# Kernel optimization log

Hardware: AMD Instinct MI355X
Metric: run time of the kernel (lower is better)

Reference implementation:

```python
import jax, jax.numpy as jnp
import numpy as np
import math

N_NODES = 4096
NUM_FEATURES = 500
NHID = 256
RATIO = 0.75


def _build_adj(x):
    # Faithful vectorization of get_threshold/get_edge_index:
    # t = 0.5 * max_{i,j} ||x_i - x_j||^2 ; directed edges (src=i -> dst=j) for j>i with d2<t.
    # Dense adjacency A[dst, src] (jit-friendly; edge count is data-dependent in the original).
    sq = jnp.sum(x * x, axis=1)
    d2 = sq[:, None] + sq[None, :] - 2.0 * (x @ x.T)  # [N,N] squared distances
    t = 0.5 * jnp.max(d2)
    N = x.shape[0]
    lower = jnp.tril(jnp.ones((N, N), dtype=bool), k=-1)  # entry [j,i], j>i
    return jnp.where(lower & (d2 < t), 1.0, 0.0).astype(x.dtype)


def _gcn(A, x, W, b):
    # PyG GCNConv: add self-loops, symmetric normalization D^-1/2 (A+I) D^-1/2, then @ (xW) + b
    N = A.shape[0]
    Ah = A + jnp.eye(N, dtype=A.dtype)
    dis = jax.lax.rsqrt(jnp.sum(Ah, axis=1))  # deg >= 1 due to self loops
    norm = (dis[:, None] * Ah) * dis[None, :]
    return norm @ (x @ W) + b


def _sag_pool(A, x, Wr, Wn, bn, k):
    # SAGPooling with default GraphConv scorer: score = sum-aggr(neighbors)@Wn + bn + x@Wr
    score = jnp.tanh(((A @ x) @ Wn + bn + x @ Wr)[:, 0])  # [N]
    vals, perm = jax.lax.top_k(score, k)  # top ceil(ratio*N) nodes, descending
    xp = x[perm] * vals[:, None]
    Ap = A[perm][:, perm]  # filter edges to surviving nodes
    return Ap, xp


def _readout(x):
    # single graph (batch=None -> all zeros): [gmp, gap] -> [1, 2*nhid]
    return jnp.concatenate([jnp.max(x, axis=0), jnp.mean(x, axis=0)])[None, :]


def setup_inputs() -> dict:
    key = jax.random.key(0)
    ks = jax.random.split(key, 16)
    s = 0.02
    inp = {
        "feature": jax.random.normal(ks[0], (N_NODES, NUM_FEATURES), jnp.float32),
        "img_info": jax.random.normal(ks[1], (N_NODES, 6), jnp.float32),
        "W_pos": jax.random.normal(ks[2], (6, 12), jnp.float32) * s,
        "b_pos": jnp.zeros((12,), jnp.float32),
        "W1": jax.random.normal(ks[3], (512, NHID), jnp.float32) * s,
        "b1": jnp.zeros((NHID,), jnp.float32),
        "W2": jax.random.normal(ks[4], (NHID, NHID), jnp.float32) * s,
        "b2": jnp.zeros((NHID,), jnp.float32),
        "W3": jax.random.normal(ks[5], (NHID, NHID), jnp.float32) * s,
        "b3": jnp.zeros((NHID,), jnp.float32),
        "Wr1": jax.random.normal(ks[6], (NHID, 1), jnp.float32) * s,
        "Wn1": jax.random.normal(ks[7], (NHID, 1), jnp.float32) * s,
        "bs1": jnp.zeros((1,), jnp.float32),
        "Wr2": jax.random.normal(ks[8], (NHID, 1), jnp.float32) * s,
        "Wn2": jax.random.normal(ks[9], (NHID, 1), jnp.float32) * s,
        "bs2": jnp.zeros((1,), jnp.float32),
        "Wr3": jax.random.normal(ks[10], (NHID, 1), jnp.float32) * s,
        "Wn3": jax.random.normal(ks[11], (NHID, 1), jnp.float32) * s,
        "bs3": jnp.zeros((1,), jnp.float32),
    }
    return inp


def reference(feature, img_info, W_pos, b_pos, W1, b1, W2, b2, W3, b3,
              Wr1, Wn1, bs1, Wr2, Wn2, bs2, Wr3, Wn3, bs3):
    pos = jax.nn.relu(img_info @ W_pos + b_pos)          # [N,12]
    feat = jnp.concatenate([feature, pos], axis=1)       # [N,512]
    N = feat.shape[0]
    k1 = math.ceil(RATIO * N)
    k2 = math.ceil(RATIO * k1)
    k3 = math.ceil(RATIO * k2)

    A = _build_adj(feat)

    x = jax.nn.relu(_gcn(A, feat, W1, b1))
    A, x = _sag_pool(A, x, Wr1, Wn1, bs1, k1)
    x1 = _readout(x)

    x = jax.nn.relu(_gcn(A, x, W2, b2))
    A, x = _sag_pool(A, x, Wr2, Wn2, bs2, k2)
    x2 = _readout(x)

    x = jax.nn.relu(_gcn(A, x, W3, b3))
    A, x = _sag_pool(A, x, Wr3, Wn3, bs3, k3)
    x3 = _readout(x)

    return x1 + x2 + x3  # [1, 2*NHID]
```

## Files before the change

kernel.cpp:

```cpp
#include <hip/hip_runtime.h>
#include <hip/hip_bf16.h>
#include <math.h>

typedef __hip_bfloat16 bf16;
typedef unsigned short ushort;
typedef unsigned int uint;
typedef unsigned long long ull;
static __device__ __forceinline__ float b2f(bf16 x){ return __bfloat162float(x); }

static __device__ __forceinline__ float ldf(const void* p, int i, int isbf){
    return isbf ? b2f(((const bf16*)p)[i]) : ((const float*)p)[i];
}
static __device__ __forceinline__ ushort f2b(float x){
    return __bfloat16_as_ushort(__float2bfloat16(x));
}
static __device__ __forceinline__ uint fcode(float v){
    uint u = __float_as_uint(v);
    return (u & 0x80000000u) ? ~u : (u | 0x80000000u);
}
static __device__ __forceinline__ float fdecode(uint c){
    uint u = (c & 0x80000000u) ? (c & 0x7FFFFFFFu) : ~c;
    return __uint_as_float(u);
}

#define NN    4096
#define FEAT0 500
#define DIN   512
#define NH    256
#define KL1   3072
#define KL2   2304
#define KL3   1728
#define EDGE_CAP 786432u

typedef __attribute__((ext_vector_type(8)))  short v8s;
typedef __attribute__((ext_vector_type(16))) float v16f;

static __device__ __forceinline__ void detect_bf16(const void* p, int n, int t,
        uint* flag){
    if (t < 256 && t < n){
        uint e = ((uint)((const ushort*)p)[t] >> 7) & 0xFFu;
        if (e >= 135u) atomicAnd(flag, 0u);
    }
}

struct DtIn { const void* p[19]; int n[19]; };
__global__ __launch_bounds__(512) void k_prep(DtIn da,
        ushort* __restrict__ Xb, float* __restrict__ sq, ushort* __restrict__ Wb,
        unsigned* __restrict__ dflag, float* __restrict__ degA,
        uint* __restrict__ maxU, float* __restrict__ sums,
        unsigned* __restrict__ ecnt, unsigned* __restrict__ maxd2,
        float* __restrict__ tmin){
    int row = blockIdx.x, t = threadIdx.x;
    if (row < NN){
        __shared__ uint fl[4];
        if (t < 4) fl[t] = 1u;
        __syncthreads();
        detect_bf16(da.p[0], da.n[0], t, &fl[0]);
        detect_bf16(da.p[1], da.n[1], t, &fl[1]);
        detect_bf16(da.p[2], da.n[2], t, &fl[2]);
        detect_bf16(da.p[3], da.n[3], t, &fl[3]);
        __syncthreads();
        int f_feat = (int)fl[0], f_img = (int)fl[1], f_wp = (int)fl[2], f_bp = (int)fl[3];
        float v;
        if (t < FEAT0) v = ldf(da.p[0], row*FEAT0 + t, f_feat);
        else {
            int c = t - FEAT0;
            float acc = ldf(da.p[3], c, f_bp);
            #pragma unroll
            for (int d = 0; d < 6; d++)
                acc += ldf(da.p[1], row*6+d, f_img) * ldf(da.p[2], d*12+c, f_wp);
            v = fmaxf(acc, 0.f);
        }
        bf16 vb = __float2bfloat16(v);
        Xb[row*DIN + t] = __bfloat16_as_ushort(vb);
        float vr = b2f(vb);
        __shared__ float red[512];
        red[t] = vr*vr;
        __syncthreads();
        for (int s = 256; s > 0; s >>= 1){ if (t < s) red[t] += red[t+s]; __syncthreads(); }
        if (t == 0) sq[row] = red[0];
    } else if (row < NN + 64){
        __shared__ uint fl[3];
        if (t < 3) fl[t] = 1u;
        __syncthreads();
        detect_bf16(da.p[4], da.n[4], t, &fl[0]);
        detect_bf16(da.p[6], da.n[6], t, &fl[1]);
        detect_bf16(da.p[8], da.n[8], t, &fl[2]);
        __syncthreads();
        int i0 = ((row - NN)*512 + t)*8;
        #pragma unroll
        for (int j = 0; j < 8; j++){
            int idx = i0 + j;
            float v;
            if (idx < 131072)       v = ldf(da.p[4], idx,          (int)fl[0]);
            else if (idx < 196608)  v = ldf(da.p[6], idx - 131072, (int)fl[1]);
            else                    v = ldf(da.p[8], idx - 196608, (int)fl[2]);
            Wb[idx] = __bfloat16_as_ushort(__float2bfloat16(v));
        }
    } else {
        for (int i = t; i < NN; i += 512) degA[i] = 1.0f;
        for (int i = t; i < 4096; i += 512) tmin[i] = INFINITY;
        for (int i = t; i < 768; i += 512){ maxU[i] = 0x007FFFFFu; sums[i] = 0.f; }
        if (t == 0){ ecnt[0]=0u; ecnt[1]=0u; ecnt[2]=0u; ecnt[3]=0u; maxd2[0]=0u; }
        if (t < 19){
            const unsigned short* h = (const unsigned short*)da.p[t];
            int n = da.n[t]; if (n > 256) n = 256;
            int isbf = 1;
            for (int j = 0; j < n; j++){
                uint e = ((uint)h[j] >> 7) & 0xFFu;
                if (e >= 135u) isbf = 0;
            }
            dflag[t] = (unsigned)isbf;
        }
    }
}

static __device__ __forceinline__ v16f mm_tile(const ushort* __restrict__ Arows,
        const ushort* __restrict__ Brows, int K, ushort* As, ushort* Bs,
        int tid, int wv, int l31, int hi){
    int row0 = tid >> 3, g0 = tid & 7;
    int row1 = row0 + 32;
    int d0 = row0*64 + ((g0^(row0&7))<<3);
    int d1 = row1*64 + ((g0^(row1&7))<<3);
    int wwr = wv >> 1, wwc = wv & 1;
    int ra0 = (wwr*32 + l31)*64, rbp = (wwc*32 + l31)*64;
    int fr7a = (wwr*32 + l31) & 7, fr7b = (wwc*32 + l31) & 7;
    float4 a0p = *(const float4*)(Arows + (size_t)row0*K + g0*8);
    float4 a1p = *(const float4*)(Arows + (size_t)row1*K + g0*8);
    float4 b0p = *(const float4*)(Brows + (size_t)row0*K + g0*8);
    float4 b1p = *(const float4*)(Brows + (size_t)row1*K + g0*8);
    v16f acc = {};
    int NC = K >> 6;
    for (int c = 0; c < NC; c++){
        __syncthreads();
        *(float4*)&As[d0] = a0p; *(float4*)&As[d1] = a1p;
        *(float4*)&Bs[d0] = b0p; *(float4*)&Bs[d1] = b1p;
        __syncthreads();
        if (c + 1 < NC){
            int k0 = (c+1)*64;
            a0p = *(const float4*)(Arows + (size_t)row0*K + k0 + g0*8);
            a1p = *(const float4*)(Arows + (size_t)row1*K + k0 + g0*8);
            b0p = *(const float4*)(Brows + (size_t)row0*K + k0 + g0*8);
            b1p = *(const float4*)(Brows + (size_t)row1*K + k0 + g0*8);
        }
        #pragma unroll
        for (int ks = 0; ks < 4; ks++){
            int gq = ks*2 + hi;
            v8s a = *(const v8s*)&As[ra0 + ((gq^fr7a)<<3)];
            v8s b = *(const v8s*)&Bs[rbp + ((gq^fr7b)<<3)];
            acc = __builtin_amdgcn_mfma_f32_32x32x16_bf16(a, b, acc, 0, 0, 0);
        }
    }
    return acc;
}

template<int PASS>
__global__ __launch_bounds__(256) void k_gram(const ushort* __restrict__ Xb,
        const float* __restrict__ sq, unsigned* __restrict__ maxd2,
        float* __restrict__ tmin, unsigned* __restrict__ ecnt,
        unsigned* __restrict__ edges, float* __restrict__ deg){
    int rb = blockIdx.x, cb = blockIdx.y;
    if (cb > rb) return;
    int tid = threadIdx.x;
    float tthr = 0.f;
    if (PASS == 2){
        tthr = 0.5f * __uint_as_float(maxd2[0]);
        if (tmin[rb*64 + cb] >= tthr) return;
    }
    __shared__ __align__(16) ushort As[64*64];
    __shared__ __align__(16) ushort Bs[64*64];
    int lane = tid & 63, wv = tid >> 6;
    int l31 = lane & 31, hi = lane >> 5;
    int wwr = wv >> 1, wwc = wv & 1;
    v16f acc = mm_tile(Xb + (size_t)rb*64*DIN, Xb + (size_t)cb*64*DIN, DIN,
                       As, Bs, tid, wv, l31, hi);
    int rbase = rb*64 + wwr*32 + 4*hi;
    int col   = cb*64 + wwc*32 + l31;
    float sqc = sq[col];
    if (PASS == 1){
        float m = 0.f, mn = INFINITY;
        #pragma unroll
        for (int i = 0; i < 16; i++){
            int r = rbase + (i&3) + 8*(i>>2);
            float d2 = sq[r] + sqc - 2.f*acc[i];
            if (r != col) m = fmaxf(m, d2);
            if (r > col)  mn = fminf(mn, d2);
        }
        #pragma unroll
        for (int off = 32; off >= 1; off >>= 1){
            m  = fmaxf(m,  __shfl_down(m,  off));
            mn = fminf(mn, __shfl_down(mn, off));
        }
        __shared__ float wmax[4], wmin[4];
        if (lane == 0){ wmax[wv] = m; wmin[wv] = mn; }
        __syncthreads();
        if (tid == 0){
            float mm = fmaxf(fmaxf(wmax[0], wmax[1]), fmaxf(wmax[2], wmax[3]));
            tmin[rb*64 + cb] = fminf(fminf(wmin[0], wmin[1]), fminf(wmin[2], wmin[3]));
            atomicMax(maxd2, __float_as_uint(fmaxf(mm, 0.f)));
        }
    } else {
        #pragma unroll
        for (int i = 0; i < 16; i++){
            int r = rbase + (i&3) + 8*(i>>2);
            float d2 = sq[r] + sqc - 2.f*acc[i];
            if (r > col && d2 < tthr){
                unsigned idx = atomicAdd(ecnt, 1u);
                if (idx < EDGE_CAP){
                    edges[idx] = ((unsigned)r << 16) | (unsigned)col;
                    atomicAdd(&deg[r], 1.0f);
                }
            }
        }
    }
}

__global__ __launch_bounds__(256) void k_xw(const ushort* __restrict__ Ab,
        const ushort* __restrict__ Wb, float* __restrict__ XW, int M, int K){
    int rb = blockIdx.x, cb = blockIdx.y;
    __shared__ __align__(16) ushort As[64*64];
    __shared__ __align__(16) ushort Bs[64*64];
    int tid = threadIdx.x, lane = tid & 63, wv = tid >> 6;
    int wwr = wv >> 1, wwc = wv & 1;
    int l31 = lane & 31, hi = lane >> 5;
    int arow0 = tid >> 3, ag = tid & 7;
    int arow1 = arow0 + 32;
    int da0 = arow0*64 + ((ag^(arow0&7))<<3);
    int da1 = arow1*64 + ((ag^(arow1&7))<<3);
    const size_t baseA = (size_t)rb*64*K;
    int kr = tid >> 2, ng = tid & 3;
    float4 a0p = *(const float4*)(Ab + baseA + (size_t)arow0*K + ag*8);
    float4 a1p = *(const float4*)(Ab + baseA + (size_t)arow1*K + ag*8);
    float4 b0p = *(const float4*)(Wb + (size_t)kr*NH + cb*64 + ng*16);
    float4 b1p = *(const float4*)(Wb + (size_t)kr*NH + cb*64 + ng*16 + 8);
    v16f acc = {};
    int ra0 = (wwr*32 + l31)*64, rbp = (wwc*32 + l31)*64;
    int fr7a = (wwr*32 + l31) & 7, fr7b = (wwc*32 + l31) & 7;
    int kg = kr >> 3, k7 = kr & 7;
    int NC = K >> 6;
    for (int c = 0; c < NC; c++){
        __syncthreads();
        *(float4*)&As[da0] = a0p; *(float4*)&As[da1] = a1p;
        const ushort* bw0 = (const ushort*)&b0p;
        const ushort* bw1 = (const ushort*)&b1p;
        #pragma unroll
        for (int j = 0; j < 8; j++){
            int nn = ng*16 + j;
            Bs[nn*64 + ((kg^(nn&7))<<3) + k7] = bw0[j];
        }
        #pragma unroll
        for (int j = 0; j < 8; j++){
            int nn = ng*16 + 8 + j;
            Bs[nn*64 + ((kg^(nn&7))<<3) + k7] = bw1[j];
        }
        __syncthreads();
        if (c + 1 < NC){
            int k0 = (c+1)*64;
            a0p = *(const float4*)(Ab + baseA + (size_t)arow0*K + k0 + ag*8);
            a1p = *(const float4*)(Ab + baseA + (size_t)arow1*K + k0 + ag*8);
            b0p = *(const float4*)(Wb + (size_t)(k0+kr)*NH + cb*64 + ng*16);
            b1p = *(const float4*)(Wb + (size_t)(k0+kr)*NH + cb*64 + ng*16 + 8);
        }
        #pragma unroll
        for (int ks = 0; ks < 4; ks++){
            int gq = ks*2 + hi;
            v8s a = *(const v8s*)&As[ra0 + ((gq^fr7a)<<3)];
            v8s b = *(const v8s*)&Bs[rbp + ((gq^fr7b)<<3)];
            acc = __builtin_amdgcn_mfma_f32_32x32x16_bf16(a, b, acc, 0, 0, 0);
        }
    }
    int n  = cb*64 + wwc*32 + l31;
    int mb = rb*64 + wwr*32 + 4*hi;
    #pragma unroll
    for (int i = 0; i < 16; i++){
        int m = mb + (i&3) + 8*(i>>2);
        XW[(size_t)m*NH + n] = acc[i];
    }
}

__global__ __launch_bounds__(256) void k_xwp(const float* __restrict__ Xn,
        const int* __restrict__ perm, const float* __restrict__ svals,
        const ushort* __restrict__ Wb, float* __restrict__ XW, int M,
        uint* __restrict__ maxU, float* __restrict__ sums, int layer){
    int rb = blockIdx.x, cb = blockIdx.y;
    __shared__ __align__(16) ushort As[64*64];
    __shared__ __align__(16) ushort Bs[64*64];
    __shared__ float pmx[256], psm[256];
    int tid = threadIdx.x, lane = tid & 63, wv = tid >> 6;
    int wwr = wv >> 1, wwc = wv & 1;
    int l31 = lane & 31, hi = lane >> 5;
    int arow0 = tid >> 3, ag = tid & 7;
    int arow1 = arow0 + 32;
    int da0 = arow0*64 + ((ag^(arow0&7))<<3);
    int da1 = arow1*64 + ((ag^(arow1&7))<<3);
    int p0 = perm[rb*64 + arow0]; float sv0 = svals[rb*64 + arow0];
    int p1 = perm[rb*64 + arow1]; float sv1 = svals[rb*64 + arow1];
    int kr = tid >> 2, ng = tid & 3;
    int kg = kr >> 3, k7 = kr & 7;
    int ra0 = (wwr*32 + l31)*64, rbp = (wwc*32 + l31)*64;
    int fr7a = (wwr*32 + l31) & 7, fr7b = (wwc*32 + l31) & 7;

    float4 xa0 = *(const float4*)(Xn + (size_t)p0*NH + ag*8);
    float4 xa1 = *(const float4*)(Xn + (size_t)p0*NH + ag*8 + 4);
    float4 xb0 = *(const float4*)(Xn + (size_t)p1*NH + ag*8);
    float4 xb1 = *(const float4*)(Xn + (size_t)p1*NH + ag*8 + 4);
    float4 wb0 = *(const float4*)(Wb + (size_t)kr*NH + cb*64 + ng*16);
    float4 wb1 = *(const float4*)(Wb + (size_t)kr*NH + cb*64 + ng*16 + 8);

    v16f acc = {};
    for (int c = 0; c < 4; c++){
        __syncthreads();
        {
            __align__(16) ushort ta[8];
            ta[0]=f2b(xa0.x*sv0); ta[1]=f2b(xa0.y*sv0); ta[2]=f2b(xa0.z*sv0); ta[3]=f2b(xa0.w*sv0);
            ta[4]=f2b(xa1.x*sv0); ta[5]=f2b(xa1.y*sv0); ta[6]=f2b(xa1.z*sv0); ta[7]=f2b(xa1.w*sv0);
            *(float4*)&As[da0] = *(const float4*)ta;
            __align__(16) ushort tb[8];
            tb[0]=f2b(xb0.x*sv1); tb[1]=f2b(xb0.y*sv1); tb[2]=f2b(xb0.z*sv1); tb[3]=f2b(xb0.w*sv1);
            tb[4]=f2b(xb1.x*sv1); tb[5]=f2b(xb1.y*sv1); tb[6]=f2b(xb1.z*sv1); tb[7]=f2b(xb1.w*sv1);
            *(float4*)&As[da1] = *(const float4*)tb;
        }
        {
            const ushort* bw0 = (const ushort*)&wb0;
            const ushort* bw1 = (const ushort*)&wb1;
            #pragma unroll
            for (int j = 0; j < 8; j++){
                int nn = ng*16 + j;
                Bs[nn*64 + ((kg^(nn&7))<<3) + k7] = bw0[j];
            }
            #pragma unroll
            for (int j = 0; j < 8; j++){
                int nn = ng*16 + 8 + j;
                Bs[nn*64 + ((kg^(nn&7))<<3) + k7] = bw1[j];
            }
        }
        __syncthreads();
        if (c < 3){
            int k0 = (c+1)*64;
            xa0 = *(const float4*)(Xn + (size_t)p0*NH + k0 + ag*8);
            xa1 = *(const float4*)(Xn + (size_t)p0*NH + k0 + ag*8 + 4);
            xb0 = *(const float4*)(Xn + (size_t)p1*NH + k0 + ag*8);
            xb1 = *(const float4*)(Xn + (size_t)p1*NH + k0 + ag*8 + 4);
            wb0 = *(const float4*)(Wb + (size_t)(k0+kr)*NH + cb*64 + ng*16);
            wb1 = *(const float4*)(Wb + (size_t)(k0+kr)*NH + cb*64 + ng*16 + 8);
        }
        if (cb == 0){
            int cc = tid & 63, q = tid >> 6;
            int gg = cc >> 3, c7 = cc & 7;
            float m = -INFINITY, s = 0.f;
            #pragma unroll
            for (int i = 0; i < 16; i++){
                int rr = q*16 + i;
                float v = __uint_as_float(((uint)As[rr*64 + ((gg^(rr&7))<<3) + c7]) << 16);
                m = fmaxf(m, v); s += v;
            }
            pmx[tid] = m; psm[tid] = s;
            __syncthreads();
            if (tid < 64){
                float mm = fmaxf(fmaxf(pmx[tid], pmx[tid+64]), fmaxf(pmx[tid+128], pmx[tid+192]));
                float ss = psm[tid] + psm[tid+64] + psm[tid+128] + psm[tid+192];
                atomicMax(&maxU[layer*NH + c*64 + tid], fcode(mm));
                atomicAdd(&sums[layer*NH + c*64 + tid], ss);
            }
        }
        #pragma unroll
        for (int ks = 0; ks < 4; ks++){
            int gq = ks*2 + hi;
            v8s a = *(const v8s*)&As[ra0 + ((gq^fr7a)<<3)];
            v8s b = *(const v8s*)&Bs[rbp + ((gq^fr7b)<<3)];
            acc = __builtin_amdgcn_mfma_f32_32x32x16_bf16(a, b, acc, 0, 0, 0);
        }
    }
    int n  = cb*64 + wwc*32 + l31;
    int mb = rb*64 + wwr*32 + 4*hi;
    #pragma unroll
    for (int i = 0; i < 16; i++){
        int m = mb + (i&3) + 8*(i>>2);
        XW[(size_t)m*NH + n] = acc[i];
    }
}

__global__ __launch_bounds__(256) void k_gcnscore(const float* __restrict__ XW,
        const unsigned* __restrict__ edges, const unsigned* __restrict__ ecnt, int slot,
        const float* __restrict__ deg, const void* __restrict__ b,
        const void* __restrict__ Wn, const void* __restrict__ Wr, const void* __restrict__ bs,
        const unsigned* __restrict__ fb, const unsigned* __restrict__ fWn,
        const unsigned* __restrict__ fWr, const unsigned* __restrict__ fbs,
        float* __restrict__ Xn, float* __restrict__ s1, float* __restrict__ z){
    int row = blockIdx.x, t = threadIdx.x;
    __shared__ unsigned eL[256];
    __shared__ unsigned Esh;
    if (t == 0){ unsigned E0 = ecnt[slot]; Esh = (E0 > EDGE_CAP) ? EDGE_CAP : E0; }
    __syncthreads();
    unsigned E = Esh;
    float disr = 1.0f / sqrtf(deg[row]);
    float acc = disr * XW[row*NH + t];
    for (unsigned base = 0; base < E; base += 256){
        unsigned nchunk = E - base; if (nchunk > 256) nchunk = 256;
        __syncthreads();
        if (t < nchunk) eL[t] = edges[base + t];
        __syncthreads();
        for (unsigned j = 0; j < nchunk; j++){
            unsigned ed = eL[j];
            if ((int)(ed >> 16) == row){
                int src = ed & 0xFFFFu;
                acc += (1.0f / sqrtf(deg[src])) * XW[src*NH + t];
            }
        }
    }
    float xn = fmaxf(fmaf(disr, acc, ldf(b, t, (int)fb[0])), 0.f);
    Xn[row*NH + t] = xn;
    float a  = xn * ldf(Wn, t, (int)fWn[0]);
    float bb = xn * ldf(Wr, t, (int)fWr[0]);
    for (int off = 32; off >= 1; off >>= 1){ a += __shfl_down(a, off); bb += __shfl_down(bb, off); }
    __shared__ float ra[4], rbv[4];
    int w = t >> 6;
    if ((t & 63) == 0){ ra[w] = a; rbv[w] = bb; }
    __syncthreads();
    if (t == 0){
        s1[row] = ra[0]+ra[1]+ra[2]+ra[3];
        z[row]  = rbv[0]+rbv[1]+rbv[2]+rbv[3] + ldf(bs, 0, (int)fbs[0]);
    }
}

__global__ __launch_bounds__(1024) void k_select(const float* __restrict__ z,
        const float* __restrict__ s1, int N, int k,
        const unsigned* __restrict__ eIn, unsigned* __restrict__ ecnt, int slotCur,
        unsigned* __restrict__ eOut, int slotOut,
        int* __restrict__ perm, float* __restrict__ svals,
        float* __restrict__ degN, int Nnext){
    __shared__ float zsh[4096];
    __shared__ int   rnk[4096];
    __shared__ uint  wcnt[16];
    __shared__ uint  wbase[16];
    __shared__ uint  sh[4];
    int t = threadIdx.x;
    int lane = t & 63, wv = t >> 6;
    for (int i = t; i < N; i += 1024){ zsh[i] = z[i]; rnk[i] = -1; }
    for (int i = t; i < Nnext; i += 1024) degN[i] = 1.0f;
    if (t == 0) sh[2] = 0u;
    __syncthreads();
    unsigned E = ecnt[slotCur]; if (E > EDGE_CAP) E = EDGE_CAP;
    for (unsigned e = t; e < E; e += 1024){
        unsigned ed = eIn[e];
        atomicAdd(&zsh[ed >> 16], s1[ed & 0xFFFFu]);
    }
    __syncthreads();
    bool v0 = t < N,        v1 = t+1024 < N,  v2 = t+2048 < N,  v3 = t+3072 < N;
    uint c0 = v0 ? fcode(zsh[t])      : 0u;
    uint c1 = v1 ? fcode(zsh[t+1024]) : 0u;
    uint c2 = v2 ? fcode(zsh[t+2048]) : 0u;
    uint c3 = v3 ? fcode(zsh[t+3072]) : 0u;
    uint T = 0u;
    for (int bit = 31; bit >= 0; bit--){
        uint cand = T | (1u << bit);
        uint c = (uint)__popcll(__ballot(v0 && c0 >= cand))
               + (uint)__popcll(__ballot(v1 && c1 >= cand))
               + (uint)__popcll(__ballot(v2 && c2 >= cand))
               + (uint)__popcll(__ballot(v3 && c3 >= cand));
        if (lane == 0) wcnt[wv] = c;
        __syncthreads();
        if (t == 0){ uint s = 0; for (int i = 0; i < 16; i++) s += wcnt[i]; sh[0] = s; }
        __syncthreads();
        if (sh[0] >= (uint)k) T = cand;
        __syncthreads();
    }
    ull b0 = __ballot(v0 && c0 > T), b1 = __ballot(v1 && c1 > T);
    ull b2 = __ballot(v2 && c2 > T), b3 = __ballot(v3 && c3 > T);
    uint t0 = (uint)__popcll(b0), t1 = (uint)__popcll(b1);
    uint t2 = (uint)__popcll(b2), t3 = (uint)__popcll(b3);
    if (lane == 0) wcnt[wv] = t0 + t1 + t2 + t3;
    __syncthreads();
    if (t == 0){
        uint s = 0;
        for (int i = 0; i < 16; i++){ wbase[i] = s; s += wcnt[i]; }
        sh[1] = s;
    }
    __syncthreads();
    uint cntGT = sh[1];
    uint rem = (uint)k - cntGT;
    ull ltm = ((ull)1 << lane) - 1;
    uint off = wbase[wv];
    if (v0 && c0 > T){ uint r = off + (uint)__popcll(b0 & ltm); int i = t;
        perm[r] = i; svals[r] = tanhf(zsh[i]); rnk[i] = (int)r; }
    off += t0;
    if (v1 && c1 > T){ uint r = off + (uint)__popcll(b1 & ltm); int i = t+1024;
        perm[r] = i; svals[r] = tanhf(zsh[i]); rnk[i] = (int)r; }
    off += t1;
    if (v2 && c2 > T){ uint r = off + (uint)__popcll(b2 & ltm); int i = t+2048;
        perm[r] = i; svals[r] = tanhf(zsh[i]); rnk[i] = (int)r; }
    off += t2;
    if (v3 && c3 > T){ uint r = off + (uint)__popcll(b3 & ltm); int i = t+3072;
        perm[r] = i; svals[r] = tanhf(zsh[i]); rnk[i] = (int)r; }
    #pragma unroll
    for (int j = 0; j < 4; j++){
        int i = t + j*1024;
        bool vv = (j==0) ? v0 : (j==1) ? v1 : (j==2) ? v2 : v3;
        uint cc = (j==0) ? c0 : (j==1) ? c1 : (j==2) ? c2 : c3;
        if (vv && cc == T){
            uint e = atomicAdd(&sh[2], 1u);
            if (e < rem){
                uint r = cntGT + e;
                perm[r] = i; svals[r] = tanhf(zsh[i]); rnk[i] = (int)r;
            }
        }
    }
    __syncthreads();
    if (slotOut >= 0){
        for (unsigned e = t; e < E; e += 1024){
            unsigned ed = eIn[e];
            int nd = rnk[ed >> 16], ns = rnk[ed & 0xFFFFu];
            if (nd >= 0 && ns >= 0){
                unsigned idx = atomicAdd(&ecnt[slotOut], 1u);
                if (idx < EDGE_CAP){
                    eOut[idx] = ((unsigned)nd << 16) | (unsigned)ns;
                    atomicAdd(&degN[nd], 1.0f);
                }
            }
        }
    }
}

__global__ __launch_bounds__(256) void k_poolread3(const float* __restrict__ Xn,
        const int* __restrict__ perm, const float* __restrict__ svals, int k,
        uint* __restrict__ maxU, float* __restrict__ sums,
        unsigned* __restrict__ done, float* __restrict__ out){
    int b = blockIdx.x, t = threadIdx.x;
    float m = -INFINITY, s = 0.f;
    for (int r = b; r < k; r += 64){
        int p = perm[r];
        float v = Xn[p*NH + t] * svals[r];
        m = fmaxf(m, v); s += v;
    }
    atomicMax(&maxU[2*NH + t], fcode(m));
    atomicAdd(&sums[2*NH + t], s);
    __threadfence();
    __shared__ uint lastv;
    if (t == 0) lastv = atomicAdd(done, 1u);
    __syncthreads();
    if (lastv == 63u){
        uint m0 = atomicAdd(&maxU[t], 0u);
        uint m1 = atomicAdd(&maxU[NH + t], 0u);
        uint m2 = atomicAdd(&maxU[2*NH + t], 0u);
        float s0 = atomicAdd(&sums[t], 0.f);
        float s1v = atomicAdd(&sums[NH + t], 0.f);
        float s2 = atomicAdd(&sums[2*NH + t], 0.f);
        out[t] = fdecode(m0) + fdecode(m1) + fdecode(m2);
        out[NH + t] = s0*(1.0f/KL1) + s1v*(1.0f/KL2) + s2*(1.0f/KL3);
    }
}

extern "C" void kernel_launch(void* const* d_in, const int* in_sizes, int n_in,
                              void* d_out, int out_size, void* d_ws, size_t ws_size,
                              hipStream_t stream)
{
    const void* b1 = d_in[5];
    const void* b2 = d_in[7];
    const void* b3 = d_in[9];
    const void* Wr1 = d_in[10]; const void* Wn1 = d_in[11]; const void* bs1 = d_in[12];
    const void* Wr2 = d_in[13]; const void* Wn2 = d_in[14]; const void* bs2 = d_in[15];
    const void* Wr3 = d_in[16]; const void* Wn3 = d_in[17]; const void* bs3 = d_in[18];

    char* w = (char*)d_ws;
    auto alloc = [&](size_t bytes)->char*{ char* p = w; w += (bytes + 255) & ~(size_t)255; return p; };
    ushort*   Xb    = (ushort*)  alloc((size_t)NN*DIN*2);
    float*    Xn    = (float*)   alloc((size_t)NN*NH*4);
    float*    XW    = (float*)   alloc((size_t)NN*NH*4);
    ushort*   Wb    = (ushort*)  alloc((size_t)262144*2);
    unsigned* E0    = (unsigned*)alloc((size_t)EDGE_CAP*4);
    unsigned* E1    = (unsigned*)alloc((size_t)EDGE_CAP*4);
    float*    tmin  = (float*)   alloc(4096*4);
    float*    sq    = (float*)   alloc(NN*4);
    float*    degA  = (float*)   alloc(NN*4);
    float*    degB  = (float*)   alloc(NN*4);
    float*    s1    = (float*)   alloc(NN*4);
    float*    z     = (float*)   alloc(NN*4);
    int*      perm  = (int*)     alloc(NN*4);
    float*    svals = (float*)   alloc(NN*4);
    unsigned* ecnt  = (unsigned*)alloc(256);
    unsigned* maxd2 = (unsigned*)alloc(256);
    unsigned* dflag = (unsigned*)alloc(256);
    uint*     maxU  = (uint*)    alloc(768*4);
    float*    sums  = (float*)   alloc(768*4);
    (void)ws_size;

    DtIn da;
    for (int i = 0; i < 19; i++){ da.p[i] = d_in[i]; da.n[i] = in_sizes[i]; }

    k_prep<<<NN + 65, 512, 0, stream>>>(da, Xb, sq, Wb, dflag, degA, maxU, sums,
            ecnt, maxd2, tmin);
    dim3 gg(64, 64);
    k_gram<1><<<gg, 256, 0, stream>>>(Xb, sq, maxd2, tmin, ecnt, E0, degA);
    k_gram<2><<<gg, 256, 0, stream>>>(Xb, sq, maxd2, tmin, ecnt, E0, degA);

    k_xw<<<dim3(64,4), 256, 0, stream>>>(Xb, Wb, XW, NN, DIN);
    k_gcnscore<<<NN, 256, 0, stream>>>(XW, E0, ecnt, 0, degA, b1, Wn1, Wr1, bs1,
            dflag+5, dflag+11, dflag+10, dflag+12, Xn, s1, z);
    k_select<<<1, 1024, 0, stream>>>(z, s1, NN, KL1, E0, ecnt, 0, E1, 1,
            perm, svals, degB, KL1);

    k_xwp<<<dim3(48,4), 256, 0, stream>>>(Xn, perm, svals, Wb + 131072, XW, KL1,
            maxU, sums, 0);
    k_gcnscore<<<KL1, 256, 0, stream>>>(XW, E1, ecnt, 1, degB, b2, Wn2, Wr2, bs2,
            dflag+7, dflag+14, dflag+13, dflag+15, Xn, s1, z);
    k_select<<<1, 1024, 0, stream>>>(z, s1, KL1, KL2, E1, ecnt, 1, E0, 2,
            perm, svals, degA, KL2);

    k_xwp<<<dim3(36,4), 256, 0, stream>>>(Xn, perm, svals, Wb + 196608, XW, KL2,
            maxU, sums, 1);
    k_gcnscore<<<KL2, 256, 0, stream>>>(XW, E0, ecnt, 2, degA, b3, Wn3, Wr3, bs3,
            dflag+9, dflag+17, dflag+16, dflag+18, Xn, s1, z);
    k_select<<<1, 1024, 0, stream>>>(z, s1, KL2, KL3, E0, ecnt, 2,
            (unsigned*)nullptr, -1, perm, svals, degB, 0);
    k_poolread3<<<64, 256, 0, stream>>>(Xn, perm, svals, KL3, maxU, sums,
            ecnt + 3, (float*)d_out);
}
```

Baseline: 263.7 us.

## Fuse X@W1 into gram pass 1 and use radix-histogram top-k select

The layer-1 feature projection (X@W1) is folded into the first gram-matrix kernel as extra grid columns, so its tiles run alongside the pairwise-distance tiles and one kernel launch disappears. Separately, the top-k threshold search in k_select swaps the 32-iteration bitwise binary search, which needs three block barriers per bit, for a three-pass radix histogram over 12, 12 and 8 bits using shared-memory atomics and a prefix scan. This trades about 96 barriers for roughly a dozen, at the cost of atomic contention on the histogram and 16 KB more shared memory.

```diff
diff --git a/kernel.cpp b/kernel.cpp
--- a/kernel.cpp
+++ b/kernel.cpp
@@ -154,72 +154,9 @@
     return acc;
 }
 
-template<int PASS>
-__global__ __launch_bounds__(256) void k_gram(const ushort* __restrict__ Xb,
-        const float* __restrict__ sq, unsigned* __restrict__ maxd2,
-        float* __restrict__ tmin, unsigned* __restrict__ ecnt,
-        unsigned* __restrict__ edges, float* __restrict__ deg){
-    int rb = blockIdx.x, cb = blockIdx.y;
-    if (cb > rb) return;
-    int tid = threadIdx.x;
-    float tthr = 0.f;
-    if (PASS == 2){
-        tthr = 0.5f * __uint_as_float(maxd2[0]);
-        if (tmin[rb*64 + cb] >= tthr) return;
-    }
-    __shared__ __align__(16) ushort As[64*64];
-    __shared__ __align__(16) ushort Bs[64*64];
-    int lane = tid & 63, wv = tid >> 6;
-    int l31 = lane & 31, hi = lane >> 5;
-    int wwr = wv >> 1, wwc = wv & 1;
-    v16f acc = mm_tile(Xb + (size_t)rb*64*DIN, Xb + (size_t)cb*64*DIN, DIN,
-                       As, Bs, tid, wv, l31, hi);
-    int rbase = rb*64 + wwr*32 + 4*hi;
-    int col   = cb*64 + wwc*32 + l31;
-    float sqc = sq[col];
-    if (PASS == 1){
-        float m = 0.f, mn = INFINITY;
-        #pragma unroll
-        for (int i = 0; i < 16; i++){
-            int r = rbase + (i&3) + 8*(i>>2);
-            float d2 = sq[r] + sqc - 2.f*acc[i];
-            if (r != col) m = fmaxf(m, d2);
-            if (r > col)  mn = fminf(mn, d2);
-        }
-        #pragma unroll
-        for (int off = 32; off >= 1; off >>= 1){
-            m  = fmaxf(m,  __shfl_down(m,  off));
-            mn = fminf(mn, __shfl_down(mn, off));
-        }
-        __shared__ float wmax[4], wmin[4];
-        if (lane == 0){ wmax[wv] = m; wmin[wv] = mn; }
-        __syncthreads();
-        if (tid == 0){
-            float mm = fmaxf(fmaxf(wmax[0], wmax[1]), fmaxf(wmax[2], wmax[3]));
-            tmin[rb*64 + cb] = fminf(fminf(wmin[0], wmin[1]), fminf(wmin[2], wmin[3]));
-            atomicMax(maxd2, __float_as_uint(fmaxf(mm, 0.f)));
-        }
-    } else {
-        #pragma unroll
-        for (int i = 0; i < 16; i++){
-            int r = rbase + (i&3) + 8*(i>>2);
-            float d2 = sq[r] + sqc - 2.f*acc[i];
-            if (r > col && d2 < tthr){
-                unsigned idx = atomicAdd(ecnt, 1u);
-                if (idx < EDGE_CAP){
-                    edges[idx] = ((unsigned)r << 16) | (unsigned)col;
-                    atomicAdd(&deg[r], 1.0f);
-                }
-            }
-        }
-    }
-}
-
-__global__ __launch_bounds__(256) void k_xw(const ushort* __restrict__ Ab,
-        const ushort* __restrict__ Wb, float* __restrict__ XW, int M, int K){
-    int rb = blockIdx.x, cb = blockIdx.y;
-    __shared__ __align__(16) ushort As[64*64];
-    __shared__ __align__(16) ushort Bs[64*64];
+static __device__ __forceinline__ void xw_body(const ushort* __restrict__ Ab,
+        const ushort* __restrict__ Wb, float* __restrict__ XW, int rb, int cb,
+        int K, ushort* As, ushort* Bs){
     int tid = threadIdx.x, lane = tid & 63, wv = tid >> 6;
     int wwr = wv >> 1, wwc = wv & 1;
     int l31 = lane & 31, hi = lane >> 5;
@@ -275,6 +212,72 @@
     for (int i = 0; i < 16; i++){
         int m = mb + (i&3) + 8*(i>>2);
         XW[(size_t)m*NH + n] = acc[i];
+    }
+}
+
+template<int PASS>
+__global__ __launch_bounds__(256) void k_gram(const ushort* __restrict__ Xb,
+        const float* __restrict__ sq, unsigned* __restrict__ maxd2,
+        float* __restrict__ tmin, unsigned* __restrict__ ecnt,
+        unsigned* __restrict__ edges, float* __restrict__ deg,
+        const ushort* __restrict__ Wb, float* __restrict__ XW){
+    __shared__ __align__(16) ushort As[64*64];
+    __shared__ __align__(16) ushort Bs[64*64];
+    int rb = blockIdx.x, cb = blockIdx.y;
+    if (PASS == 1 && cb >= 64){
+        xw_body(Xb, Wb, XW, rb, cb - 64, DIN, As, Bs);
+        return;
+    }
+    if (cb > rb) return;
+    int tid = threadIdx.x;
+    float tthr = 0.f;
+    if (PASS == 2){
+        tthr = 0.5f * __uint_as_float(maxd2[0]);
+        if (tmin[rb*64 + cb] >= tthr) return;
+    }
+    int lane = tid & 63, wv = tid >> 6;
+    int l31 = lane & 31, hi = lane >> 5;
+    int wwr = wv >> 1, wwc = wv & 1;
+    v16f acc = mm_tile(Xb + (size_t)rb*64*DIN, Xb + (size_t)cb*64*DIN, DIN,
+                       As, Bs, tid, wv, l31, hi);
+    int rbase = rb*64 + wwr*32 + 4*hi;
+    int col   = cb*64 + wwc*32 + l31;
+    float sqc = sq[col];
+    if (PASS == 1){
+        float m = 0.f, mn = INFINITY;
+        #pragma unroll
+        for (int i = 0; i < 16; i++){
+            int r = rbase + (i&3) + 8*(i>>2);
+            float d2 = sq[r] + sqc - 2.f*acc[i];
+            if (r != col) m = fmaxf(m, d2);
+            if (r > col)  mn = fminf(mn, d2);
+        }
+        #pragma unroll
+        for (int off = 32; off >= 1; off >>= 1){
+            m  = fmaxf(m,  __shfl_down(m,  off));
+            mn = fminf(mn, __shfl_down(mn, off));
+        }
+        __shared__ float wmax[4], wmin[4];
+        if (lane == 0){ wmax[wv] = m; wmin[wv] = mn; }
+        __syncthreads();
+        if (tid == 0){
+            float mm = fmaxf(fmaxf(wmax[0], wmax[1]), fmaxf(wmax[2], wmax[3]));
+            tmin[rb*64 + cb] = fminf(fminf(wmin[0], wmin[1]), fminf(wmin[2], wmin[3]));
+            atomicMax(maxd2, __float_as_uint(fmaxf(mm, 0.f)));
+        }
+    } else {
+        #pragma unroll
+        for (int i = 0; i < 16; i++){
+            int r = rbase + (i&3) + 8*(i>>2);
+            float d2 = sq[r] + sqc - 2.f*acc[i];
+            if (r > col && d2 < tthr){
+                unsigned idx = atomicAdd(ecnt, 1u);
+                if (idx < EDGE_CAP){
+                    edges[idx] = ((unsigned)r << 16) | (unsigned)col;
+                    atomicAdd(&deg[r], 1.0f);
+                }
+            }
+        }
     }
 }
 
@@ -423,6 +426,37 @@
     }
 }
 
+static __device__ __forceinline__ uint2 radix_scan(const uint* hist, uint* wt,
+        uint* ws, uint* sh, int t, int lane, int wv, uint kk, int NB){
+    uint loc = 0;
+    int b0 = t << 2;
+    if (b0 < NB) loc = hist[b0] + hist[b0+1] + hist[b0+2] + hist[b0+3];
+    uint s = loc;
+    #pragma unroll
+    for (int off = 1; off < 64; off <<= 1){
+        uint u = __shfl_down(s, off);
+        if (lane + off < 64) s += u;
+    }
+    if (lane == 0) wt[wv] = s;
+    __syncthreads();
+    if (t < 16){
+        uint a = 0;
+        for (int j = t + 1; j < 16; j++) a += wt[j];
+        ws[t] = a;
+    }
+    __syncthreads();
+    if (b0 < NB){
+        uint run = ws[wv] + (s - loc);
+        for (int b = b0 + 3; b >= b0; b--){
+            uint h = hist[b];
+            if (run < kk && run + h >= kk){ sh[0] = (uint)b; sh[1] = run; }
+            run += h;
+        }
+    }
+    __syncthreads();
+    return make_uint2(sh[0], sh[1]);
+}
+
 __global__ __launch_bounds__(1024) void k_select(const float* __restrict__ z,
         const float* __restrict__ s1, int N, int k,
         const unsigned* __restrict__ eIn, unsigned* __restrict__ ecnt, int slotCur,
@@ -431,6 +465,7 @@
         float* __restrict__ degN, int Nnext){
     __shared__ float zsh[4096];
     __shared__ int   rnk[4096];
+    __shared__ uint  hist[4096];
     __shared__ uint  wcnt[16];
     __shared__ uint  wbase[16];
     __shared__ uint  sh[4];
@@ -451,20 +486,36 @@
     uint c1 = v1 ? fcode(zsh[t+1024]) : 0u;
     uint c2 = v2 ? fcode(zsh[t+2048]) : 0u;
     uint c3 = v3 ? fcode(zsh[t+3072]) : 0u;
-    uint T = 0u;
-    for (int bit = 31; bit >= 0; bit--){
-        uint cand = T | (1u << bit);
-        uint c = (uint)__popcll(__ballot(v0 && c0 >= cand))
-               + (uint)__popcll(__ballot(v1 && c1 >= cand))
-               + (uint)__popcll(__ballot(v2 && c2 >= cand))
-               + (uint)__popcll(__ballot(v3 && c3 >= cand));
-        if (lane == 0) wcnt[wv] = c;
-        __syncthreads();
-        if (t == 0){ uint s = 0; for (int i = 0; i < 16; i++) s += wcnt[i]; sh[0] = s; }
-        __syncthreads();
-        if (sh[0] >= (uint)k) T = cand;
-        __syncthreads();
-    }
+
+    for (int i = t; i < 4096; i += 1024) hist[i] = 0u;
+    __syncthreads();
+    if (v0) atomicAdd(&hist[c0 >> 20], 1u);
+    if (v1) atomicAdd(&hist[c1 >> 20], 1u);
+    if (v2) atomicAdd(&hist[c2 >> 20], 1u);
+    if (v3) atomicAdd(&hist[c3 >> 20], 1u);
+    __syncthreads();
+    uint2 p1 = radix_scan(hist, wcnt, wbase, sh, t, lane, wv, (uint)k, 4096);
+    uint B1 = p1.x; uint kk2 = (uint)k - p1.y;
+    for (int i = t; i < 4096; i += 1024) hist[i] = 0u;
+    __syncthreads();
+    if (v0 && (c0 >> 20) == B1) atomicAdd(&hist[(c0 >> 8) & 0xFFFu], 1u);
+    if (v1 && (c1 >> 20) == B1) atomicAdd(&hist[(c1 >> 8) & 0xFFFu], 1u);
+    if (v2 && (c2 >> 20) == B1) atomicAdd(&hist[(c2 >> 8) & 0xFFFu], 1u);
+    if (v3 && (c3 >> 20) == B1) atomicAdd(&hist[(c3 >> 8) & 0xFFFu], 1u);
+    __syncthreads();
+    uint2 p2 = radix_scan(hist, wcnt, wbase, sh, t, lane, wv, kk2, 4096);
+    uint B2 = p2.x; uint kk3 = kk2 - p2.y;
+    uint hi24 = (B1 << 12) | B2;
+    for (int i = t; i < 256; i += 1024) hist[i] = 0u;
+    __syncthreads();
+    if (v0 && (c0 >> 8) == hi24) atomicAdd(&hist[c0 & 0xFFu], 1u);
+    if (v1 && (c1 >> 8) == hi24) atomicAdd(&hist[c1 & 0xFFu], 1u);
+    if (v2 && (c2 >> 8) == hi24) atomicAdd(&hist[c2 & 0xFFu], 1u);
+    if (v3 && (c3 >> 8) == hi24) atomicAdd(&hist[c3 & 0xFFu], 1u);
+    __syncthreads();
+    uint2 p3 = radix_scan(hist, wcnt, wbase, sh, t, lane, wv, kk3, 256);
+    uint T = (B1 << 20) | (B2 << 8) | p3.x;
+
     ull b0 = __ballot(v0 && c0 > T), b1 = __ballot(v1 && c1 > T);
     ull b2 = __ballot(v2 && c2 > T), b3 = __ballot(v3 && c3 > T);
     uint t0 = (uint)__popcll(b0), t1 = (uint)__popcll(b1);
@@ -589,11 +640,11 @@
 
     k_prep<<<NN + 65, 512, 0, stream>>>(da, Xb, sq, Wb, dflag, degA, maxU, sums,
             ecnt, maxd2, tmin);
-    dim3 gg(64, 64);
-    k_gram<1><<<gg, 256, 0, stream>>>(Xb, sq, maxd2, tmin, ecnt, E0, degA);
-    k_gram<2><<<gg, 256, 0, stream>>>(Xb, sq, maxd2, tmin, ecnt, E0, degA);
-
-    k_xw<<<dim3(64,4), 256, 0, stream>>>(Xb, Wb, XW, NN, DIN);
+    k_gram<1><<<dim3(64,68), 256, 0, stream>>>(Xb, sq, maxd2, tmin, ecnt, E0, degA,
+            Wb, XW);
+    k_gram<2><<<dim3(64,64), 256, 0, stream>>>(Xb, sq, maxd2, tmin, ecnt, E0, degA,
+            Wb, XW);
+
     k_gcnscore<<<NN, 256, 0, stream>>>(XW, E0, ecnt, 0, degA, b1, Wn1, Wr1, bs1,
             dflag+5, dflag+11, dflag+10, dflag+12, Xn, s1, z);
     k_select<<<1, 1024, 0, stream>>>(z, s1, NN, KL1, E0, ecnt, 0, E1, 1,
```

Result: faster. 236.8 us (-10.2%).
